# Optimization experiments

Hardware: AMD Instinct MI355X
Metric: run time of the kernel (lower is better)

Reference implementation:

```python
import jax, jax.numpy as jnp
import numpy as np

N = 50000
C = 128
E = 800000
STEPS = 3


def setup_inputs() -> dict:
    key = jax.random.key(0)
    ks = jax.random.split(key, 8)
    x = jax.random.normal(ks[0], (N, C), dtype=jnp.float32)
    edge_index = jax.random.randint(ks[1], (2, E), 0, N, dtype=jnp.int64)
    s = 1.0 / np.sqrt(C)
    W_lin = jax.random.uniform(ks[2], (C, C), jnp.float32, -s, s)   # nn.Linear(C, C, bias=False)
    W_ih = jax.random.uniform(ks[3], (3 * C, C), jnp.float32, -s, s)  # GRUCell weight_ih
    W_hh = jax.random.uniform(ks[4], (3 * C, C), jnp.float32, -s, s)  # GRUCell weight_hh
    b_ih = jax.random.uniform(ks[5], (3 * C,), jnp.float32, -s, s)
    b_hh = jax.random.uniform(ks[6], (3 * C,), jnp.float32, -s, s)
    return {"x": x, "edge_index": edge_index, "W_lin": W_lin,
            "W_ih": W_ih, "W_hh": W_hh, "b_ih": b_ih, "b_hh": b_hh}


def _gru_cell(inp, h, W_ih, W_hh, b_ih, b_hh):
    # torch.nn.GRUCell math
    gi = inp @ W_ih.T + b_ih   # [N, 3C]
    gh = h @ W_hh.T + b_hh     # [N, 3C]
    i_r, i_z, i_n = jnp.split(gi, 3, axis=-1)
    h_r, h_z, h_n = jnp.split(gh, 3, axis=-1)
    r = jax.nn.sigmoid(i_r + h_r)
    z = jax.nn.sigmoid(i_z + h_z)
    n = jnp.tanh(i_n + r * h_n)
    return (1.0 - z) * n + z * h


def reference(x, edge_index, W_lin, W_ih, W_hh, b_ih, b_hh):
    src = edge_index[0]
    dst = edge_index[1]
    state = x
    for _ in range(STEPS):
        m = state @ W_lin.T                       # [N, C] dense transform
        msgs = jnp.take(m, src, axis=0)           # [E, C] gather
        propagated = jax.ops.segment_sum(msgs, dst, num_segments=N)  # scatter-add
        state = _gru_cell(propagated, state, W_ih, W_hh, b_ih, b_hh)
    return state
```

## Files before the change

kernel.cpp:

```cpp
#include <hip/hip_runtime.h>

#define NN 50000
#define CC 128
#define EE 800000
#define NT 1563
#define NBLK 196

typedef short bf16x8 __attribute__((ext_vector_type(8)));
typedef float f32x4 __attribute__((ext_vector_type(4)));

__device__ __forceinline__ float bf2f(unsigned int u16) {
  union { unsigned int u; float f; } x; x.u = u16 << 16; return x.f;
}
__device__ __forceinline__ unsigned short f2bf(float f) {
  union { float f; unsigned int u; } x; x.f = f;
  unsigned int u = x.u;
  unsigned int r = (u + 0x7fffu + ((u >> 16) & 1u)) >> 16;
  return (unsigned short)r;
}
__device__ __forceinline__ float fsigmoid(float x) {
  return __fdividef(1.f, 1.f + __expf(-x));
}
__device__ __forceinline__ float ftanh(float x) {
  return 1.f - __fdividef(2.f, 1.f + __expf(2.f * x));
}

__global__ void cast_f2b_k(const float* __restrict__ in, unsigned short* __restrict__ out, int n4) {
  int i = blockIdx.x * blockDim.x + threadIdx.x;
  int stride = gridDim.x * blockDim.x;
  for (; i < n4; i += stride) {
    float4 v = ((const float4*)in)[i];
    ushort4 o;
    o.x = f2bf(v.x); o.y = f2bf(v.y); o.z = f2bf(v.z); o.w = f2bf(v.w);
    ((ushort4*)out)[i] = o;
  }
}

__global__ __launch_bounds__(256) void wprep_k(const float* __restrict__ Wih,
                                               const float* __restrict__ Wlin,
                                               const float* __restrict__ Whh,
                                               unsigned short* __restrict__ Wcb,
                                               unsigned short* __restrict__ Whhb) {
  if (blockIdx.x < 192) {
    int gid = blockIdx.x * 256 + threadIdx.x;
    int i = gid >> 7, j = gid & 127;
    float acc = 0.f;
    #pragma unroll 8
    for (int k = 0; k < 128; ++k)
      acc += Wih[i * 128 + k] * Wlin[k * 128 + j];
    Wcb[i * 128 + j] = f2bf(acc);
  } else {
    int i = (blockIdx.x - 192) * 256 + threadIdx.x;
    float4 v = ((const float4*)Whh)[i];
    ushort4 o;
    o.x = f2bf(v.x); o.y = f2bf(v.y); o.z = f2bf(v.z); o.w = f2bf(v.w);
    ((ushort4*)Whhb)[i] = o;
  }
}

__global__ void zero_k(int* __restrict__ p, int n) {
  int i = blockIdx.x * blockDim.x + threadIdx.x;
  if (i < n) p[i] = 0;
}

__global__ void hist_k(const int* __restrict__ dst, int* __restrict__ cnt,
                       int* __restrict__ rank, int n4) {
  int i = blockIdx.x * blockDim.x + threadIdx.x;
  if (i < n4) {
    int4 d = ((const int4*)dst)[i];
    int4 r;
    r.x = atomicAdd(&cnt[d.x], 1);
    r.y = atomicAdd(&cnt[d.y], 1);
    r.z = atomicAdd(&cnt[d.z], 1);
    r.w = atomicAdd(&cnt[d.w], 1);
    ((int4*)rank)[i] = r;
  }
}

__global__ __launch_bounds__(256) void scan1_k(const int* __restrict__ cnt,
                                               int* __restrict__ rowptr,
                                               int* __restrict__ bsum, int N) {
  __shared__ int wtot[4];
  int tid = threadIdx.x, lane = tid & 63, w = tid >> 6;
  int i = blockIdx.x * 256 + tid;
  int v = (i < N) ? cnt[i] : 0;
  int x = v;
  #pragma unroll
  for (int off = 1; off < 64; off <<= 1) {
    int t = __shfl_up(x, off, 64);
    if (lane >= off) x += t;
  }
  if (lane == 63) wtot[w] = x;
  __syncthreads();
  int woff = 0;
  for (int j = 0; j < w; ++j) woff += wtot[j];
  int excl = x - v + woff;
  if (i < N) rowptr[i] = excl;
  if (tid == 255) bsum[blockIdx.x] = excl + v;
}

__global__ __launch_bounds__(256) void scan2_k(int* __restrict__ bsum, int* __restrict__ rowptr, int NB) {
  __shared__ int wtot[4];
  int tid = threadIdx.x, lane = tid & 63, w = tid >> 6;
  int v = (tid < NB) ? bsum[tid] : 0;
  int x = v;
  #pragma unroll
  for (int off = 1; off < 64; off <<= 1) {
    int t = __shfl_up(x, off, 64);
    if (lane >= off) x += t;
  }
  if (lane == 63) wtot[w] = x;
  __syncthreads();
  int woff = 0;
  for (int j = 0; j < w; ++j) woff += wtot[j];
  int excl = x - v + woff;
  if (tid < NB) bsum[tid] = excl;
  if (tid == 255) rowptr[NN] = excl + v;
}

__global__ void scan3_k(int* __restrict__ rowptr, const int* __restrict__ bsum, int N) {
  int i = blockIdx.x * 256 + threadIdx.x;
  if (i < N) rowptr[i] = rowptr[i] + bsum[i >> 8];
}

__global__ void fill_k(const int* __restrict__ src, const int* __restrict__ dst,
                       const int* __restrict__ rank, const int* __restrict__ rowptr,
                       int* __restrict__ colx, int n4) {
  int i = blockIdx.x * blockDim.x + threadIdx.x;
  if (i < n4) {
    int4 s = ((const int4*)src)[i];
    int4 d = ((const int4*)dst)[i];
    int4 r = ((const int4*)rank)[i];
    colx[rowptr[d.x] + r.x] = s.x;
    colx[rowptr[d.y] + r.y] = s.y;
    colx[rowptr[d.z] + r.z] = s.z;
    colx[rowptr[d.w] + r.w] = s.w;
  }
}

__global__ __launch_bounds__(256) void agg2_k(const unsigned short* __restrict__ M,
                                              const int* __restrict__ rowptr,
                                              const int* __restrict__ colx,
                                              unsigned short* __restrict__ P, int N) {
  int wid = (blockIdx.x * 256 + threadIdx.x) >> 6;
  int lane = threadIdx.x & 63;
  if (wid >= N) return;
  int beg = rowptr[wid], end = rowptr[wid + 1];
  int half = lane >> 5, li = lane & 31;
  float a0 = 0.f, a1 = 0.f, a2 = 0.f, a3 = 0.f;
  int n = end - beg;
  int i = 0;
  for (; i + 8 <= n; i += 8) {
    int e = beg + i + half;
    int s0 = colx[e], s1 = colx[e + 2], s2 = colx[e + 4], s3 = colx[e + 6];
    uint2 v0 = *(const uint2*)(M + s0 * CC + li * 4);
    uint2 v1 = *(const uint2*)(M + s1 * CC + li * 4);
    uint2 v2 = *(const uint2*)(M + s2 * CC + li * 4);
    uint2 v3 = *(const uint2*)(M + s3 * CC + li * 4);
    a0 += bf2f(v0.x & 0xffffu); a1 += bf2f(v0.x >> 16); a2 += bf2f(v0.y & 0xffffu); a3 += bf2f(v0.y >> 16);
    a0 += bf2f(v1.x & 0xffffu); a1 += bf2f(v1.x >> 16); a2 += bf2f(v1.y & 0xffffu); a3 += bf2f(v1.y >> 16);
    a0 += bf2f(v2.x & 0xffffu); a1 += bf2f(v2.x >> 16); a2 += bf2f(v2.y & 0xffffu); a3 += bf2f(v2.y >> 16);
    a0 += bf2f(v3.x & 0xffffu); a1 += bf2f(v3.x >> 16); a2 += bf2f(v3.y & 0xffffu); a3 += bf2f(v3.y >> 16);
  }
  for (; i + 2 <= n; i += 2) {
    int e = beg + i + half;
    int s = colx[e];
    uint2 v = *(const uint2*)(M + s * CC + li * 4);
    a0 += bf2f(v.x & 0xffffu); a1 += bf2f(v.x >> 16); a2 += bf2f(v.y & 0xffffu); a3 += bf2f(v.y >> 16);
  }
  if (i < n && half == 0) {
    int s = colx[beg + i];
    uint2 v = *(const uint2*)(M + s * CC + li * 4);
    a0 += bf2f(v.x & 0xffffu); a1 += bf2f(v.x >> 16); a2 += bf2f(v.y & 0xffffu); a3 += bf2f(v.y >> 16);
  }
  a0 += __shfl_xor(a0, 32, 64);
  a1 += __shfl_xor(a1, 32, 64);
  a2 += __shfl_xor(a2, 32, 64);
  a3 += __shfl_xor(a3, 32, 64);
  if (half == 0) {
    uint2 o;
    o.x = (unsigned int)f2bf(a0) | ((unsigned int)f2bf(a1) << 16);
    o.y = (unsigned int)f2bf(a2) | ((unsigned int)f2bf(a3) << 16);
    *(uint2*)(P + wid * CC + li * 4) = o;
  }
}

__global__ __launch_bounds__(256, 2) void gru3_k(const unsigned short* __restrict__ Pb,
                                                 const unsigned short* __restrict__ Sb_in,
                                                 unsigned short* __restrict__ Sb_out,
                                                 const float* __restrict__ h_in,
                                                 float* __restrict__ h_out,
                                                 const unsigned short* __restrict__ Wcb,
                                                 const unsigned short* __restrict__ Whhb,
                                                 const float* __restrict__ bih,
                                                 const float* __restrict__ bhh) {
  __shared__ unsigned short sA[2][2][32][128];
  const int tid = threadIdx.x;
  const int half = blockIdx.x & 1;
  const int group = blockIdx.x >> 1;
  const int lane = tid & 63, w = tid >> 6;
  const int l15 = lane & 15, l4 = lane >> 4;

  const int c_loc = w * 16 + l15;
  const int cg = half * 64 + c_loc;

  bf16x8 Breg[6][4];
  #pragma unroll
  for (int pi = 0; pi < 6; ++pi) {
    const unsigned short* Wm = (pi < 3) ? Wcb : Whhb;
    int p = (pi < 3) ? pi : pi - 3;
    const unsigned short* base = Wm + (p * 128 + cg) * 128 + l4 * 8;
    #pragma unroll
    for (int ks = 0; ks < 4; ++ks)
      Breg[pi][ks] = *(const bf16x8*)(base + ks * 32);
  }

  const float bir = bih[cg], biz = bih[cg + 128], bin_ = bih[cg + 256];
  const float bhr = bhh[cg], bhz = bhh[cg + 128], bhn = bhh[cg + 256];

  auto loadA = [&](int t, uint4* r) {
    int rowbase = t * 32;
    #pragma unroll
    for (int k = 0; k < 4; ++k) {
      int idx = k * 256 + tid;
      int mat = idx >> 9, j = idx & 511, row = j >> 4, ch = j & 15;
      int grow = rowbase + row;
      const unsigned short* srcp = mat ? Sb_in : Pb;
      r[k] = (grow < NN) ? *(const uint4*)(srcp + grow * 128 + ch * 8) : make_uint4(0, 0, 0, 0);
    }
  };
  auto writeA = [&](int buf, const uint4* r) {
    #pragma unroll
    for (int k = 0; k < 4; ++k) {
      int idx = k * 256 + tid;
      int mat = idx >> 9, j = idx & 511, row = j >> 4, ch = j & 15;
      *(uint4*)&sA[buf][mat][row][((ch ^ (row & 15)) * 8)] = r[k];
    }
  };

  uint4 pre[4];
  int t0 = group;
  loadA(t0, pre);
  writeA(0, pre);
  int cur = 0;
  for (int t = t0; t < NT; t += 256) {
    __syncthreads();
    int tn = t + 256;
    uint4 nxt[4];
    if (tn < NT) loadA(tn, nxt);

    f32x4 acc[6][2] = {};
    #pragma unroll
    for (int ks = 0; ks < 4; ++ks) {
      bf16x8 a[2][2];
      #pragma unroll
      for (int mat = 0; mat < 2; ++mat)
        #pragma unroll
        for (int rt = 0; rt < 2; ++rt) {
          int row = rt * 16 + l15;
          a[mat][rt] = *(const bf16x8*)&sA[cur][mat][row][(((ks * 4 + l4) ^ l15) * 8)];
        }
      #pragma unroll
      for (int pi = 0; pi < 6; ++pi) {
        int am = (pi < 3) ? 0 : 1;
        acc[pi][0] = __builtin_amdgcn_mfma_f32_16x16x32_bf16(a[am][0], Breg[pi][ks], acc[pi][0], 0, 0, 0);
        acc[pi][1] = __builtin_amdgcn_mfma_f32_16x16x32_bf16(a[am][1], Breg[pi][ks], acc[pi][1], 0, 0, 0);
      }
    }

    int rowbase = t * 32;
    #pragma unroll
    for (int rt = 0; rt < 2; ++rt)
      #pragma unroll
      for (int i = 0; i < 4; ++i) {
        int row = rowbase + rt * 16 + l4 * 4 + i;
        if (row < NN) {
          float gir = acc[0][rt][i] + bir;
          float giz = acc[1][rt][i] + biz;
          float gin = acc[2][rt][i] + bin_;
          float ghr = acc[3][rt][i] + bhr;
          float ghz = acc[4][rt][i] + bhz;
          float ghn = acc[5][rt][i] + bhn;
          float r = fsigmoid(gir + ghr);
          float z = fsigmoid(giz + ghz);
          float n = ftanh(gin + r * ghn);
          float h = h_in[row * 128 + cg];
          float o = n + z * (h - n);
          h_out[row * 128 + cg] = o;
          Sb_out[row * 128 + cg] = f2bf(o);
        }
      }
    if (tn < NT) writeA(cur ^ 1, nxt);
    cur ^= 1;
  }
}

extern "C" void kernel_launch(void* const* d_in, const int* in_sizes, int n_in,
                              void* d_out, int out_size, void* d_ws, size_t ws_size,
                              hipStream_t stream) {
  const float* x    = (const float*)d_in[0];
  const int*   ei   = (const int*)d_in[1];
  const float* Wlin = (const float*)d_in[2];
  const float* Wih  = (const float*)d_in[3];
  const float* Whh  = (const float*)d_in[4];
  const float* bih  = (const float*)d_in[5];
  const float* bhh  = (const float*)d_in[6];
  float* out = (float*)d_out;

  char* ws = (char*)d_ws;
  size_t off = 0;
  auto alloc = [&](size_t bytes) -> void* {
    void* p = ws + off;
    off += (bytes + 255) & ~(size_t)255;
    return p;
  };
  unsigned short* SbA  = (unsigned short*)alloc((size_t)NN * CC * 2);
  unsigned short* SbB  = (unsigned short*)alloc((size_t)NN * CC * 2);
  unsigned short* Prb  = (unsigned short*)alloc((size_t)NN * CC * 2);
  float*          Sf   = (float*)alloc((size_t)NN * CC * 4);
  unsigned short* Wcb  = (unsigned short*)alloc((size_t)3 * CC * CC * 2);
  unsigned short* Whhb = (unsigned short*)alloc((size_t)3 * CC * CC * 2);
  int* rowptr = (int*)alloc((size_t)(NN + 1) * 4);
  int* cnt    = (int*)alloc((size_t)NN * 4);
  int* rank   = (int*)alloc((size_t)EE * 4);
  int* colx   = (int*)alloc((size_t)EE * 4);
  int* bsum   = (int*)alloc(256 * 4);

  const int* srcI = ei;
  const int* dstI = ei + EE;

  cast_f2b_k<<<1024, 256, 0, stream>>>(x, SbA, NN * CC / 4);
  wprep_k<<<240, 256, 0, stream>>>(Wih, Wlin, Whh, Wcb, Whhb);

  zero_k<<<NBLK, 256, 0, stream>>>(cnt, NN);
  hist_k<<<(EE / 4 + 255) / 256, 256, 0, stream>>>(dstI, cnt, rank, EE / 4);
  scan1_k<<<NBLK, 256, 0, stream>>>(cnt, rowptr, bsum, NN);
  scan2_k<<<1, 256, 0, stream>>>(bsum, rowptr, NBLK);
  scan3_k<<<NBLK, 256, 0, stream>>>(rowptr, bsum, NN);
  fill_k<<<(EE / 4 + 255) / 256, 256, 0, stream>>>(srcI, dstI, rank, rowptr, colx, EE / 4);

  const int aggBlocks = (NN + 3) / 4;

  agg2_k<<<aggBlocks, 256, 0, stream>>>(SbA, rowptr, colx, Prb, NN);
  gru3_k<<<512, 256, 0, stream>>>(Prb, SbA, SbB, x, Sf, Wcb, Whhb, bih, bhh);
  agg2_k<<<aggBlocks, 256, 0, stream>>>(SbB, rowptr, colx, Prb, NN);
  gru3_k<<<512, 256, 0, stream>>>(Prb, SbB, SbA, Sf, Sf, Wcb, Whhb, bih, bhh);
  agg2_k<<<aggBlocks, 256, 0, stream>>>(SbA, rowptr, colx, Prb, NN);
  gru3_k<<<512, 256, 0, stream>>>(Prb, SbA, SbB, Sf, out, Wcb, Whhb, bih, bhh);
}
```

Baseline: 344.8 us.

## Merge GRU column halves into one block and read hidden state from bf16 tile

The GRU kernel now uses 512-thread blocks that cover all 128 output columns, instead of two 256-thread blocks that each loaded the same 32-row A tile. This halves redundant global loads of the P and S tiles. The fp32 hidden-state buffer is removed: h is read from the bf16 state tile already in shared memory, and only the final step writes fp32. This lowers precision of the carried state (h now round-trips through bf16 each step), and the hist kernel is simplified to scalar per-edge atomics.

```diff
diff --git a/kernel.cpp b/kernel.cpp
--- a/kernel.cpp
+++ b/kernel.cpp
@@ -64,17 +64,9 @@
 }
 
 __global__ void hist_k(const int* __restrict__ dst, int* __restrict__ cnt,
-                       int* __restrict__ rank, int n4) {
+                       int* __restrict__ rank, int n) {
   int i = blockIdx.x * blockDim.x + threadIdx.x;
-  if (i < n4) {
-    int4 d = ((const int4*)dst)[i];
-    int4 r;
-    r.x = atomicAdd(&cnt[d.x], 1);
-    r.y = atomicAdd(&cnt[d.y], 1);
-    r.z = atomicAdd(&cnt[d.z], 1);
-    r.w = atomicAdd(&cnt[d.w], 1);
-    ((int4*)rank)[i] = r;
-  }
+  if (i < n) rank[i] = atomicAdd(&cnt[dst[i]], 1);
 }
 
 __global__ __launch_bounds__(256) void scan1_k(const int* __restrict__ cnt,
@@ -185,24 +177,20 @@
   }
 }
 
-__global__ __launch_bounds__(256, 2) void gru3_k(const unsigned short* __restrict__ Pb,
+__global__ __launch_bounds__(512, 2) void gru4_k(const unsigned short* __restrict__ Pb,
                                                  const unsigned short* __restrict__ Sb_in,
                                                  unsigned short* __restrict__ Sb_out,
-                                                 const float* __restrict__ h_in,
-                                                 float* __restrict__ h_out,
+                                                 float* __restrict__ fout,
                                                  const unsigned short* __restrict__ Wcb,
                                                  const unsigned short* __restrict__ Whhb,
                                                  const float* __restrict__ bih,
                                                  const float* __restrict__ bhh) {
   __shared__ unsigned short sA[2][2][32][128];
   const int tid = threadIdx.x;
-  const int half = blockIdx.x & 1;
-  const int group = blockIdx.x >> 1;
   const int lane = tid & 63, w = tid >> 6;
   const int l15 = lane & 15, l4 = lane >> 4;
 
-  const int c_loc = w * 16 + l15;
-  const int cg = half * 64 + c_loc;
+  const int cg = w * 16 + l15;
 
   bf16x8 Breg[6][4];
   #pragma unroll
@@ -221,8 +209,8 @@
   auto loadA = [&](int t, uint4* r) {
     int rowbase = t * 32;
     #pragma unroll
-    for (int k = 0; k < 4; ++k) {
-      int idx = k * 256 + tid;
+    for (int k = 0; k < 2; ++k) {
+      int idx = k * 512 + tid;
       int mat = idx >> 9, j = idx & 511, row = j >> 4, ch = j & 15;
       int grow = rowbase + row;
       const unsigned short* srcp = mat ? Sb_in : Pb;
@@ -231,22 +219,22 @@
   };
   auto writeA = [&](int buf, const uint4* r) {
     #pragma unroll
-    for (int k = 0; k < 4; ++k) {
-      int idx = k * 256 + tid;
+    for (int k = 0; k < 2; ++k) {
+      int idx = k * 512 + tid;
       int mat = idx >> 9, j = idx & 511, row = j >> 4, ch = j & 15;
       *(uint4*)&sA[buf][mat][row][((ch ^ (row & 15)) * 8)] = r[k];
     }
   };
 
-  uint4 pre[4];
-  int t0 = group;
+  uint4 pre[2];
+  int t0 = blockIdx.x;
   loadA(t0, pre);
   writeA(0, pre);
   int cur = 0;
   for (int t = t0; t < NT; t += 256) {
     __syncthreads();
     int tn = t + 256;
-    uint4 nxt[4];
+    uint4 nxt[2];
     if (tn < NT) loadA(tn, nxt);
 
     f32x4 acc[6][2] = {};
@@ -273,7 +261,8 @@
     for (int rt = 0; rt < 2; ++rt)
       #pragma unroll
       for (int i = 0; i < 4; ++i) {
-        int row = rowbase + rt * 16 + l4 * 4 + i;
+        int row_loc = rt * 16 + l4 * 4 + i;
+        int row = rowbase + row_loc;
         if (row < NN) {
           float gir = acc[0][rt][i] + bir;
           float giz = acc[1][rt][i] + biz;
@@ -284,10 +273,10 @@
           float r = fsigmoid(gir + ghr);
           float z = fsigmoid(giz + ghz);
           float n = ftanh(gin + r * ghn);
-          float h = h_in[row * 128 + cg];
+          float h = bf2f((unsigned int)sA[cur][1][row_loc][(((cg >> 3) ^ (row_loc & 15)) << 3) + (cg & 7)]);
           float o = n + z * (h - n);
-          h_out[row * 128 + cg] = o;
-          Sb_out[row * 128 + cg] = f2bf(o);
+          if (fout) fout[row * 128 + cg] = o;
+          else      Sb_out[row * 128 + cg] = f2bf(o);
         }
       }
     if (tn < NT) writeA(cur ^ 1, nxt);
@@ -317,7 +306,6 @@
   unsigned short* SbA  = (unsigned short*)alloc((size_t)NN * CC * 2);
   unsigned short* SbB  = (unsigned short*)alloc((size_t)NN * CC * 2);
   unsigned short* Prb  = (unsigned short*)alloc((size_t)NN * CC * 2);
-  float*          Sf   = (float*)alloc((size_t)NN * CC * 4);
   unsigned short* Wcb  = (unsigned short*)alloc((size_t)3 * CC * CC * 2);
   unsigned short* Whhb = (unsigned short*)alloc((size_t)3 * CC * CC * 2);
   int* rowptr = (int*)alloc((size_t)(NN + 1) * 4);
@@ -333,7 +321,7 @@
   wprep_k<<<240, 256, 0, stream>>>(Wih, Wlin, Whh, Wcb, Whhb);
 
   zero_k<<<NBLK, 256, 0, stream>>>(cnt, NN);
-  hist_k<<<(EE / 4 + 255) / 256, 256, 0, stream>>>(dstI, cnt, rank, EE / 4);
+  hist_k<<<EE / 256, 256, 0, stream>>>(dstI, cnt, rank, EE);
   scan1_k<<<NBLK, 256, 0, stream>>>(cnt, rowptr, bsum, NN);
   scan2_k<<<1, 256, 0, stream>>>(bsum, rowptr, NBLK);
   scan3_k<<<NBLK, 256, 0, stream>>>(rowptr, bsum, NN);
@@ -342,9 +330,9 @@
   const int aggBlocks = (NN + 3) / 4;
 
   agg2_k<<<aggBlocks, 256, 0, stream>>>(SbA, rowptr, colx, Prb, NN);
-  gru3_k<<<512, 256, 0, stream>>>(Prb, SbA, SbB, x, Sf, Wcb, Whhb, bih, bhh);
+  gru4_k<<<256, 512, 0, stream>>>(Prb, SbA, SbB, nullptr, Wcb, Whhb, bih, bhh);
   agg2_k<<<aggBlocks, 256, 0, stream>>>(SbB, rowptr, colx, Prb, NN);
-  gru3_k<<<512, 256, 0, stream>>>(Prb, SbB, SbA, Sf, Sf, Wcb, Whhb, bih, bhh);
+  gru4_k<<<256, 512, 0, stream>>>(Prb, SbB, SbA, nullptr, Wcb, Whhb, bih, bhh);
   agg2_k<<<aggBlocks, 256, 0, stream>>>(SbA, rowptr, colx, Prb, NN);
-  gru3_k<<<512, 256, 0, stream>>>(Prb, SbA, SbB, Sf, out, Wcb, Whhb, bih, bhh);
-}
+  gru4_k<<<256, 512, 0, stream>>>(Prb, SbA, SbB, out, Wcb, Whhb, bih, bhh);
+}
```

Result: faster. 336.0 us (-2.5%).
